# Kernel optimization log

Hardware: AMD Instinct MI355X
Metric: run time of the kernel (lower is better)

## Reference

```python
import jax, jax.numpy as jnp
import numpy as np

N_NODES = 100000
N_EDGES = 1600000
IN_DIM, HID_DIM, OUT_DIM = 64, 64, 32
NEG_SLOPE = 0.2


def _gat_conv(x, W, att_src, att_dst, b, src, dst, n_nodes):
    # x: [N, Din], W: [Din, Dout], att_src/att_dst: [Dout], b: [Dout]
    h = x @ W                                   # [N, Dout]
    a_s = h @ att_src                           # [N] per-source-node score
    a_d = h @ att_dst                           # [N] per-dest-node score
    e = jax.nn.leaky_relu(a_s[src] + a_d[dst], NEG_SLOPE)  # [E]
    # numerically stable segment softmax over edges grouped by dst
    e_max = jax.ops.segment_max(e, dst, num_segments=n_nodes)
    w = jnp.exp(e - e_max[dst])
    denom = jax.ops.segment_sum(w, dst, num_segments=n_nodes)
    alpha = w / denom[dst]                      # [E]
    out = jax.ops.segment_sum(alpha[:, None] * h[src], dst, num_segments=n_nodes)
    return out + b


def setup_inputs() -> dict:
    key = jax.random.key(0)
    ks = jax.random.split(key, 10)
    x = jax.random.normal(ks[0], (N_NODES, IN_DIM), dtype=jnp.float32)
    edge_index = jax.random.randint(ks[1], (2, N_EDGES), 0, N_NODES, dtype=jnp.int64)
    s1 = 1.0 / np.sqrt(IN_DIM)
    s2 = 1.0 / np.sqrt(HID_DIM)
    return {
        "x": x,
        "edge_index": edge_index,
        "W1": jax.random.normal(ks[2], (IN_DIM, HID_DIM), dtype=jnp.float32) * s1,
        "att_src1": jax.random.normal(ks[3], (HID_DIM,), dtype=jnp.float32) * s2,
        "att_dst1": jax.random.normal(ks[4], (HID_DIM,), dtype=jnp.float32) * s2,
        "b1": jnp.zeros((HID_DIM,), dtype=jnp.float32),
        "W2": jax.random.normal(ks[5], (HID_DIM, OUT_DIM), dtype=jnp.float32) * s2,
        "att_src2": jax.random.normal(ks[6], (OUT_DIM,), dtype=jnp.float32) * (1.0 / np.sqrt(OUT_DIM)),
        "att_dst2": jax.random.normal(ks[7], (OUT_DIM,), dtype=jnp.float32) * (1.0 / np.sqrt(OUT_DIM)),
        "b2": jnp.zeros((OUT_DIM,), dtype=jnp.float32),
    }


def reference(x, edge_index, W1, att_src1, att_dst1, b1, W2, att_src2, att_dst2, b2):
    n = x.shape[0]
    # PyG GATConv default add_self_loops=True
    loops = jnp.arange(n, dtype=edge_index.dtype)
    src = jnp.concatenate([edge_index[0], loops])
    dst = jnp.concatenate([edge_index[1], loops])
    h = _gat_conv(x, W1, att_src1, att_dst1, b1, src, dst, n)
    h = jax.nn.relu(h)
    h = _gat_conv(h, W2, att_src2, att_dst2, b2, src, dst, n)
    return jnp.tanh(h)
```

## Files before the change

### kernel.cpp

```cpp
#include <hip/hip_runtime.h>
#include <cmath>


__device__ __forceinline__ float lrelu(float e) { return e >= 0.f ? e : 0.2f * e; }


__global__ void zero_bcnt(int* __restrict__ bcnt, int NFB) {
  int i = blockIdx.x * 256 + threadIdx.x;
  if (i < NFB) bcnt[i] = 0;
}

__global__ void bucket_scatter(const int* __restrict__ src, const int* __restrict__ dst,
                               int* __restrict__ bcnt, unsigned int* __restrict__ bucket,
                               int E, int CAP) {
  int i = blockIdx.x * 256 + threadIdx.x;
  if (i >= E) return;
  int s = src[i];
  int d = dst[i];
  int f = d >> 4;
  int pos = atomicAdd(&bcnt[f], 1);
  if (pos < CAP)
    bucket[(size_t)f * CAP + pos] = ((unsigned int)s << 9) | (unsigned int)(d & 511);
}

__global__ void scan_buckets(const int* __restrict__ bcnt, int* __restrict__ cbase,
                             int* __restrict__ row_off, int NBKC, int NFB, int N, int Etot) {
  __shared__ int s[256];
  int tid = threadIdx.x;
  int csum = 0;
  if (tid < NBKC) {
    int f0 = tid * 32;
    for (int j = 0; j < 32; j++) {
      int f = f0 + j;
      if (f < NFB) csum += bcnt[f];
    }
    int nodes = N - tid * 512;
    csum += (nodes > 512) ? 512 : nodes;
  }
  s[tid] = csum;
  __syncthreads();
  #pragma unroll
  for (int off = 1; off < 256; off <<= 1) {
    int t = (tid >= off) ? s[tid - off] : 0;
    __syncthreads();
    s[tid] += t;
    __syncthreads();
  }
  if (tid < NBKC) cbase[tid] = s[tid] - csum;
  if (tid == 0) row_off[N] = Etot;
}

__global__ __launch_bounds__(256) void bucket_csr(
    const unsigned int* __restrict__ bucket, const int* __restrict__ bcnt,
    const int* __restrict__ cbase, int* __restrict__ row_off,
    int* __restrict__ csr_src, int N, int NFB, int CAP) {
  __shared__ int hist[512];
  __shared__ int lscan[512];
  __shared__ int cur[512];
  __shared__ int ssum[256];
  int b = blockIdx.x;
  int tid = threadIdx.x;
  int base = cbase[b];

  hist[tid]       = (b * 512 + tid < N) ? 1 : 0;
  hist[tid + 256] = (b * 512 + tid + 256 < N) ? 1 : 0;
  cur[tid] = 0; cur[tid + 256] = 0;
  __syncthreads();

  for (int j = 0; j < 32; j++) {
    int f = b * 32 + j;
    if (f >= NFB) break;
    int c = bcnt[f]; if (c > CAP) c = CAP;
    const unsigned int* items = bucket + (size_t)f * CAP;
    for (int i = tid; i < c; i += 256)
      atomicAdd(&hist[items[i] & 511], 1);
  }
  __syncthreads();

  int a0 = hist[2 * tid], a1 = hist[2 * tid + 1];
  ssum[tid] = a0 + a1;
  __syncthreads();
  #pragma unroll
  for (int off = 1; off < 256; off <<= 1) {
    int t = (tid >= off) ? ssum[tid - off] : 0;
    __syncthreads();
    ssum[tid] += t;
    __syncthreads();
  }
  int excl = ssum[tid] - (a0 + a1);
  lscan[2 * tid] = excl;
  lscan[2 * tid + 1] = excl + a0;

  int v = b * 512 + 2 * tid;
  if (v < N)     row_off[v]     = base + excl;
  if (v + 1 < N) row_off[v + 1] = base + excl + a0;
  __syncthreads();

  for (int j = 0; j < 32; j++) {
    int f = b * 32 + j;
    if (f >= NFB) break;
    int c = bcnt[f]; if (c > CAP) c = CAP;
    const unsigned int* items = bucket + (size_t)f * CAP;
    for (int i = tid; i < c; i += 256) {
      unsigned int r = items[i];
      int ld = (int)(r & 511);
      int pos = base + lscan[ld] + atomicAdd(&cur[ld], 1);
      csr_src[pos] = (int)(r >> 9);
    }
  }
  __syncthreads();

  #pragma unroll
  for (int half = 0; half < 2; half++) {
    int lv = tid + half * 256;
    int gv = b * 512 + lv;
    if (gv < N) csr_src[base + lscan[lv] + cur[lv]] = gv;
  }
}

template <int DIN, int DOUT>
__global__ __launch_bounds__(256) void gemm_scores(
    const float* __restrict__ x, const float* __restrict__ W,
    const float* __restrict__ att_s, const float* __restrict__ att_d,
    float* __restrict__ h, float* __restrict__ a_s, float* __restrict__ a_d, int N) {
  constexpr int TPR = DOUT / 4;
  constexpr int ROWS = 256 / TPR;
  constexpr int XPAD = 4;
  __shared__ float Ws[DIN * DOUT];
  __shared__ float xs[ROWS * (DIN + XPAD)];
  int tid = threadIdx.x;
  for (int i = tid; i < DIN * DOUT / 4; i += 256)
    ((float4*)Ws)[i] = ((const float4*)W)[i];
  int row0 = blockIdx.x * ROWS;
  for (int i = tid; i < ROWS * DIN / 4; i += 256) {
    int r = (i * 4) / DIN;
    int k = (i * 4) % DIN;
    int grow = row0 + r;
    float4 vv = (grow < N) ? ((const float4*)x)[((size_t)grow * DIN + k) / 4]
                           : make_float4(0.f, 0.f, 0.f, 0.f);
    *(float4*)&xs[r * (DIN + XPAD) + k] = vv;
  }
  __syncthreads();

  int rl = tid / TPR;
  int c0 = (tid % TPR) * 4;
  int row = row0 + rl;
  float4 acc = make_float4(0.f, 0.f, 0.f, 0.f);
  #pragma unroll
  for (int k = 0; k < DIN; k += 4) {
    float4 xv = *(const float4*)&xs[rl * (DIN + XPAD) + k];
    float4 w0 = *(const float4*)&Ws[(k + 0) * DOUT + c0];
    float4 w1 = *(const float4*)&Ws[(k + 1) * DOUT + c0];
    float4 w2 = *(const float4*)&Ws[(k + 2) * DOUT + c0];
    float4 w3 = *(const float4*)&Ws[(k + 3) * DOUT + c0];
    acc.x += xv.x * w0.x; acc.y += xv.x * w0.y; acc.z += xv.x * w0.z; acc.w += xv.x * w0.w;
    acc.x += xv.y * w1.x; acc.y += xv.y * w1.y; acc.z += xv.y * w1.z; acc.w += xv.y * w1.w;
    acc.x += xv.z * w2.x; acc.y += xv.z * w2.y; acc.z += xv.z * w2.z; acc.w += xv.z * w2.w;
    acc.x += xv.w * w3.x; acc.y += xv.w * w3.y; acc.z += xv.w * w3.z; acc.w += xv.w * w3.w;
  }
  float4 as4 = *(const float4*)&att_s[c0];
  float4 ad4 = *(const float4*)&att_d[c0];
  float ps = acc.x * as4.x + acc.y * as4.y + acc.z * as4.z + acc.w * as4.w;
  float pd = acc.x * ad4.x + acc.y * ad4.y + acc.z * ad4.z + acc.w * ad4.w;
  #pragma unroll
  for (int mask = TPR / 2; mask >= 1; mask >>= 1) {
    ps += __shfl_xor(ps, mask);
    pd += __shfl_xor(pd, mask);
  }
  if (row < N) {
    *(float4*)&h[(size_t)row * DOUT + c0] = acc;
    if ((tid % TPR) == 0) { a_s[row] = ps; a_d[row] = pd; }
  }
}

template <int D, bool RELU>
__global__ __launch_bounds__(256) void aggregate(
    const float* __restrict__ h, const float* __restrict__ a_s, const float* __restrict__ a_d,
    const int* __restrict__ row_off, const int* __restrict__ csr_src,
    const float* __restrict__ bias, float* __restrict__ out, int N) {
  constexpr int QL = D / 4;
  constexpr int NPW = 64 / QL;
  constexpr int B = 8;
  int wave = (int)((blockIdx.x * (size_t)blockDim.x + threadIdx.x) >> 6);
  int lane = threadIdx.x & 63;
  int q = lane / QL;
  int p = lane % QL;
  int v = wave * NPW + q;
  bool active = v < N;
  int vv = active ? v : (N - 1);

  int beg = row_off[vv];
  int end = row_off[vv + 1];
  float adv = a_d[vv];
  float4 bias4 = *(const float4*)&bias[p * 4];

  float4 acc = make_float4(0.f, 0.f, 0.f, 0.f);
  float den = 0.f;

  for (int k0 = beg; k0 < end; k0 += B) {
    int  s[B];
    bool g[B];
    float ev[B];
    float4 hv[B];
    #pragma unroll
    for (int j = 0; j < B; j++) {
      g[j] = (k0 + j) < end;
      s[j] = g[j] ? csr_src[k0 + j] : 0;
    }
    #pragma unroll
    for (int j = 0; j < B; j++) ev[j] = a_s[s[j]];
    #pragma unroll
    for (int j = 0; j < B; j++) hv[j] = *(const float4*)&h[(size_t)s[j] * D + p * 4];
    #pragma unroll
    for (int j = 0; j < B; j++) {
      float w = g[j] ? __expf(lrelu(ev[j] + adv)) : 0.f;
      acc.x += w * hv[j].x;
      acc.y += w * hv[j].y;
      acc.z += w * hv[j].z;
      acc.w += w * hv[j].w;
      den += w;
    }
  }

  if (active) {
    float inv = 1.f / den;
    float4 o;
    o.x = acc.x * inv + bias4.x;
    o.y = acc.y * inv + bias4.y;
    o.z = acc.z * inv + bias4.z;
    o.w = acc.w * inv + bias4.w;
    if (RELU) {
      o.x = fmaxf(o.x, 0.f); o.y = fmaxf(o.y, 0.f);
      o.z = fmaxf(o.z, 0.f); o.w = fmaxf(o.w, 0.f);
    } else {
      o.x = tanhf(o.x); o.y = tanhf(o.y);
      o.z = tanhf(o.z); o.w = tanhf(o.w);
    }
    *(float4*)&out[(size_t)v * D + p * 4] = o;
  }
}


extern "C" void kernel_launch(void* const* d_in, const int* in_sizes, int n_in,
                              void* d_out, int out_size, void* d_ws, size_t ws_size,
                              hipStream_t stream) {
  const float* x    = (const float*)d_in[0];
  const int*   ei   = (const int*)d_in[1];
  const float* W1   = (const float*)d_in[2];
  const float* as1v = (const float*)d_in[3];
  const float* ad1v = (const float*)d_in[4];
  const float* b1   = (const float*)d_in[5];
  const float* W2   = (const float*)d_in[6];
  const float* as2v = (const float*)d_in[7];
  const float* ad2v = (const float*)d_in[8];
  const float* b2   = (const float*)d_in[9];
  float* out = (float*)d_out;

  const int N = in_sizes[0] / 64;
  const int E = in_sizes[1] / 2;
  const int Etot = E + N;
  const int* src = ei;
  const int* dst = ei + E;

  const int NFB  = (N + 15) / 16;
  const int NBKC = (N + 511) / 512;
  const int CAP  = (E / NFB) * 5 / 4 + 64;

  char* ws = (char*)d_ws;
  size_t off = 0;
  auto alloc = [&](size_t bytes) -> void* {
    void* p = ws + off;
    off = (off + bytes + 255) & ~(size_t)255;
    return p;
  };
  float* h1      = (float*)alloc((size_t)N * 64 * sizeof(float));
  float* out1    = (float*)alloc((size_t)N * 64 * sizeof(float));
  float* a_s1    = (float*)alloc((size_t)N * sizeof(float));
  float* a_d1    = (float*)alloc((size_t)N * sizeof(float));
  float* a_s2    = (float*)alloc((size_t)N * sizeof(float));
  float* a_d2    = (float*)alloc((size_t)N * sizeof(float));
  int*   bcnt    = (int*)alloc((size_t)NFB * sizeof(int));
  int*   cbase   = (int*)alloc(((size_t)NBKC + 1) * sizeof(int));
  int*   row_off = (int*)alloc(((size_t)N + 1) * sizeof(int));
  int*   csr_src = (int*)alloc(((size_t)Etot + 16) * sizeof(int));
  unsigned int* bucket = (unsigned int*)alloc((size_t)NFB * CAP * sizeof(unsigned int));
  (void)ws_size; (void)n_in; (void)out_size;

  zero_bcnt<<<(NFB + 255) / 256, 256, 0, stream>>>(bcnt, NFB);
  bucket_scatter<<<(E + 255) / 256, 256, 0, stream>>>(src, dst, bcnt, bucket, E, CAP);
  scan_buckets<<<1, 256, 0, stream>>>(bcnt, cbase, row_off, NBKC, NFB, N, Etot);
  bucket_csr<<<NBKC, 256, 0, stream>>>(bucket, bcnt, cbase, row_off, csr_src, N, NFB, CAP);

  gemm_scores<64, 64><<<(N + 15) / 16, 256, 0, stream>>>(x, W1, as1v, ad1v, h1, a_s1, a_d1, N);
  {
    int waves = (N + 3) / 4;
    int blocks = (waves + 3) / 4;
    aggregate<64, true><<<blocks, 256, 0, stream>>>(h1, a_s1, a_d1, row_off, csr_src, b1, out1, N);
  }
  gemm_scores<64, 32><<<(N + 31) / 32, 256, 0, stream>>>(out1, W2, as2v, ad2v, h1, a_s2, a_d2, N);
  {
    int waves = (N + 7) / 8;
    int blocks = (waves + 3) / 4;
    aggregate<32, false><<<blocks, 256, 0, stream>>>(h1, a_s2, a_d2, row_off, csr_src, b2, out, N);
  }
}
```

Baseline: 340.0 us.

## Stage edge bucketing in shared memory with coarse 512-node buckets

Replaces the per-edge global-atomic scatter into 16-node fine buckets with a block-level staging pass. Each block bins 4096 edges into shared-memory bins keyed by 512-node bucket, then flushes each bin with one global atomic and a run of writes. The CSR build then reads one contiguous bucket per block. This is meant to cut global atomic contention and scattered writes. In exchange it adds shared-memory pressure (about 50KB per block, limiting occupancy), a global fallback path for bins that overflow, and serial per-thread flush loops that write uncoalesced.

```diff
diff --git a/kernel.cpp b/kernel.cpp
--- a/kernel.cpp
+++ b/kernel.cpp
@@ -5,35 +5,60 @@
 __device__ __forceinline__ float lrelu(float e) { return e >= 0.f ? e : 0.2f * e; }
 
 
-__global__ void zero_bcnt(int* __restrict__ bcnt, int NFB) {
+__global__ void zero_gcnt(int* __restrict__ gcnt, int NBKC) {
   int i = blockIdx.x * 256 + threadIdx.x;
-  if (i < NFB) bcnt[i] = 0;
-}
-
-__global__ void bucket_scatter(const int* __restrict__ src, const int* __restrict__ dst,
-                               int* __restrict__ bcnt, unsigned int* __restrict__ bucket,
-                               int E, int CAP) {
-  int i = blockIdx.x * 256 + threadIdx.x;
-  if (i >= E) return;
-  int s = src[i];
-  int d = dst[i];
-  int f = d >> 4;
-  int pos = atomicAdd(&bcnt[f], 1);
-  if (pos < CAP)
-    bucket[(size_t)f * CAP + pos] = ((unsigned int)s << 9) | (unsigned int)(d & 511);
-}
-
-__global__ void scan_buckets(const int* __restrict__ bcnt, int* __restrict__ cbase,
-                             int* __restrict__ row_off, int NBKC, int NFB, int N, int Etot) {
+  if (i < NBKC) gcnt[i] = 0;
+}
+
+#define BCAP 48
+__global__ __launch_bounds__(256) void stage_scatter(
+    const int* __restrict__ src, const int* __restrict__ dst,
+    int* __restrict__ gcnt, unsigned int* __restrict__ bucket,
+    int E, int CAP, int NBKC) {
+  __shared__ unsigned int bin[256][BCAP + 1];
+  __shared__ int bc[256];
+  for (int chunk = blockIdx.x * 4096; chunk < E; chunk += gridDim.x * 4096) {
+    bc[threadIdx.x] = 0;
+    __syncthreads();
+    #pragma unroll
+    for (int k = 0; k < 16; ++k) {
+      int i = chunk + k * 256 + threadIdx.x;
+      if (i < E) {
+        int s = src[i], d = dst[i];
+        int b = d >> 9;
+        unsigned int rec = ((unsigned int)s << 9) | (unsigned int)(d & 511);
+        int pos = atomicAdd(&bc[b], 1);
+        if (pos < BCAP) {
+          bin[b][pos] = rec;
+        } else {
+          int gpos = atomicAdd(&gcnt[b], 1);
+          if (gpos < CAP) bucket[(size_t)b * CAP + gpos] = rec;
+        }
+      }
+    }
+    __syncthreads();
+    int b = threadIdx.x;
+    if (b < NBKC) {
+      int cnt = bc[b]; if (cnt > BCAP) cnt = BCAP;
+      if (cnt > 0) {
+        int base = atomicAdd(&gcnt[b], cnt);
+        for (int j = 0; j < cnt; ++j) {
+          int gpos = base + j;
+          if (gpos < CAP) bucket[(size_t)b * CAP + gpos] = bin[b][j];
+        }
+      }
+    }
+    __syncthreads();
+  }
+}
+
+__global__ void scan_buckets(const int* __restrict__ gcnt, int* __restrict__ cbase,
+                             int* __restrict__ row_off, int NBKC, int N, int Etot) {
   __shared__ int s[256];
   int tid = threadIdx.x;
   int csum = 0;
   if (tid < NBKC) {
-    int f0 = tid * 32;
-    for (int j = 0; j < 32; j++) {
-      int f = f0 + j;
-      if (f < NFB) csum += bcnt[f];
-    }
+    csum = gcnt[tid];
     int nodes = N - tid * 512;
     csum += (nodes > 512) ? 512 : nodes;
   }
@@ -51,9 +76,9 @@
 }
 
 __global__ __launch_bounds__(256) void bucket_csr(
-    const unsigned int* __restrict__ bucket, const int* __restrict__ bcnt,
+    const unsigned int* __restrict__ bucket, const int* __restrict__ gcnt,
     const int* __restrict__ cbase, int* __restrict__ row_off,
-    int* __restrict__ csr_src, int N, int NFB, int CAP) {
+    int* __restrict__ csr_src, int N, int CAP) {
   __shared__ int hist[512];
   __shared__ int lscan[512];
   __shared__ int cur[512];
@@ -61,20 +86,16 @@
   int b = blockIdx.x;
   int tid = threadIdx.x;
   int base = cbase[b];
+  int cnt = gcnt[b]; if (cnt > CAP) cnt = CAP;
+  const unsigned int* items = bucket + (size_t)b * CAP;
 
   hist[tid]       = (b * 512 + tid < N) ? 1 : 0;
   hist[tid + 256] = (b * 512 + tid + 256 < N) ? 1 : 0;
   cur[tid] = 0; cur[tid + 256] = 0;
   __syncthreads();
 
-  for (int j = 0; j < 32; j++) {
-    int f = b * 32 + j;
-    if (f >= NFB) break;
-    int c = bcnt[f]; if (c > CAP) c = CAP;
-    const unsigned int* items = bucket + (size_t)f * CAP;
-    for (int i = tid; i < c; i += 256)
-      atomicAdd(&hist[items[i] & 511], 1);
-  }
+  for (int i = tid; i < cnt; i += 256)
+    atomicAdd(&hist[items[i] & 511], 1);
   __syncthreads();
 
   int a0 = hist[2 * tid], a1 = hist[2 * tid + 1];
@@ -96,17 +117,11 @@
   if (v + 1 < N) row_off[v + 1] = base + excl + a0;
   __syncthreads();
 
-  for (int j = 0; j < 32; j++) {
-    int f = b * 32 + j;
-    if (f >= NFB) break;
-    int c = bcnt[f]; if (c > CAP) c = CAP;
-    const unsigned int* items = bucket + (size_t)f * CAP;
-    for (int i = tid; i < c; i += 256) {
-      unsigned int r = items[i];
-      int ld = (int)(r & 511);
-      int pos = base + lscan[ld] + atomicAdd(&cur[ld], 1);
-      csr_src[pos] = (int)(r >> 9);
-    }
+  for (int i = tid; i < cnt; i += 256) {
+    unsigned int r = items[i];
+    int ld = (int)(r & 511);
+    int pos = base + lscan[ld] + atomicAdd(&cur[ld], 1);
+    csr_src[pos] = (int)(r >> 9);
   }
   __syncthreads();
 
@@ -262,9 +277,8 @@
   const int* src = ei;
   const int* dst = ei + E;
 
-  const int NFB  = (N + 15) / 16;
   const int NBKC = (N + 511) / 512;
-  const int CAP  = (E / NFB) * 5 / 4 + 64;
+  const int CAP  = (E / NBKC) * 5 / 4 + 512;
 
   char* ws = (char*)d_ws;
   size_t off = 0;
@@ -279,17 +293,21 @@
   float* a_d1    = (float*)alloc((size_t)N * sizeof(float));
   float* a_s2    = (float*)alloc((size_t)N * sizeof(float));
   float* a_d2    = (float*)alloc((size_t)N * sizeof(float));
-  int*   bcnt    = (int*)alloc((size_t)NFB * sizeof(int));
+  int*   gcnt    = (int*)alloc((size_t)NBKC * sizeof(int));
   int*   cbase   = (int*)alloc(((size_t)NBKC + 1) * sizeof(int));
   int*   row_off = (int*)alloc(((size_t)N + 1) * sizeof(int));
   int*   csr_src = (int*)alloc(((size_t)Etot + 16) * sizeof(int));
-  unsigned int* bucket = (unsigned int*)alloc((size_t)NFB * CAP * sizeof(unsigned int));
+  unsigned int* bucket = (unsigned int*)alloc((size_t)NBKC * CAP * sizeof(unsigned int));
   (void)ws_size; (void)n_in; (void)out_size;
 
-  zero_bcnt<<<(NFB + 255) / 256, 256, 0, stream>>>(bcnt, NFB);
-  bucket_scatter<<<(E + 255) / 256, 256, 0, stream>>>(src, dst, bcnt, bucket, E, CAP);
-  scan_buckets<<<1, 256, 0, stream>>>(bcnt, cbase, row_off, NBKC, NFB, N, Etot);
-  bucket_csr<<<NBKC, 256, 0, stream>>>(bucket, bcnt, cbase, row_off, csr_src, N, NFB, CAP);
+  zero_gcnt<<<(NBKC + 255) / 256, 256, 0, stream>>>(gcnt, NBKC);
+  {
+    int blocks = (E + 4095) / 4096;
+    if (blocks > 2048) blocks = 2048;
+    stage_scatter<<<blocks, 256, 0, stream>>>(src, dst, gcnt, bucket, E, CAP, NBKC);
+  }
+  scan_buckets<<<1, 256, 0, stream>>>(gcnt, cbase, row_off, NBKC, N, Etot);
+  bucket_csr<<<NBKC, 256, 0, stream>>>(bucket, gcnt, cbase, row_off, csr_src, N, CAP);
 
   gemm_scores<64, 64><<<(N + 15) / 16, 256, 0, stream>>>(x, W1, as1v, ad1v, h1, a_s1, a_d1, N);
   {
```

Result: faster. 272.3 us (-19.9%).
